# Optimization experiments

Measured on AMD Instinct MI355X. Metric: run time of the kernel, lower is better.

The kernel has to match this reference:

```python
import jax, jax.numpy as jnp
import numpy as np

B, L = 2, 2048          # batch, seq len (self-attention: M == L)
H, D, NB = 8, 16, 8     # n_heads, clifford_dim, n_blades (2^3 for sig_g=[1,1,1])
DM = H * D * NB         # d_model = 1024

# reverse() signs per blade for a 3D algebra, blade grades [0,1,1,1,2,2,2,3]:
# (-1)^{k(k-1)/2}; Euclidean metric signs from get_blade_signs are all +1,
# so the combined twist q_w = reverse(q) * signs is just these per-blade signs.
REV_SIGNS = jnp.array([1., 1., 1., 1., -1., -1., -1., -1.], dtype=jnp.float32)


def setup_inputs() -> dict:
    key = jax.random.key(0)
    ks = jax.random.split(key, 7)
    s = 1.0 / np.sqrt(DM)
    return {
        "query": jax.random.normal(ks[0], (B, L, DM), dtype=jnp.float32),
        "Wq": jax.random.normal(ks[1], (DM, DM), dtype=jnp.float32) * s,
        "bq": jax.random.normal(ks[2], (DM,), dtype=jnp.float32) * s,
        "Wk": jax.random.normal(ks[3], (DM, DM), dtype=jnp.float32) * s,
        "bk": jax.random.normal(ks[4], (DM,), dtype=jnp.float32) * s,
        "Wv": jax.random.normal(ks[5], (DM, DM), dtype=jnp.float32) * s,
        "bv": jax.random.normal(ks[6], (DM,), dtype=jnp.float32) * s,
    }


def reference(query, Wq, bq, Wk, bk, Wv, bv):
    b, l, _ = query.shape
    # projections (torch Linear: x @ W^T + b), reshape to (B,H,L,D,NB)
    def proj(x, W, bias):
        y = x @ W.T + bias
        return y.reshape(b, l, H, D, NB).transpose(0, 2, 1, 3, 4)

    q = proj(query, Wq, bq)
    k = proj(query, Wk, bk)   # self-attention: key = value = query
    v = proj(query, Wv, bv)

    q_w = q * REV_SIGNS  # reverse + blade-sign twist (elementwise over blade axis)
    scale = 1.0 / np.sqrt(D * NB)
    logits = jnp.einsum('bhldi,bhmdi->bhlm', q_w, k) * scale
    attn = jax.nn.softmax(logits, axis=-1)
    out = jnp.einsum('bhlm,bhmdi->bhldi', attn, v)
    out = out.transpose(0, 2, 1, 3, 4).reshape(b, l, -1)
    return out, attn.mean(axis=1)  # need_weights=True path
```

## Files before the change

kernel.cpp:

```cpp
#include <hip/hip_runtime.h>

typedef __attribute__((ext_vector_type(8))) __bf16 bf16x8;
typedef __attribute__((ext_vector_type(4))) __bf16 bf16x4;
typedef __attribute__((ext_vector_type(4))) float f32x4;
typedef __attribute__((ext_vector_type(16))) float f32x16;
typedef __attribute__((ext_vector_type(8))) unsigned short us8;
typedef __attribute__((ext_vector_type(4))) unsigned int u32x4;

constexpr float SCALE_L2E = 0.08838834764831845f * 1.4426950408889634f;

__device__ __forceinline__ unsigned short f2bf(float f) {
  unsigned int u = __float_as_uint(f);
  u = (u + 0x7FFFu + ((u >> 16) & 1u)) >> 16;
  return (unsigned short)u;
}

__device__ __forceinline__ void gl_lds16(const void* g, void* l) {
  __builtin_amdgcn_global_load_lds(
      (__attribute__((address_space(1))) void*)const_cast<void*>(g),
      (__attribute__((address_space(3))) void*)l, 16, 0, 0);
}

__global__ __launch_bounds__(256) void k_convert(
    const float* __restrict__ q, const float* __restrict__ wq,
    const float* __restrict__ wk, const float* __restrict__ wv,
    unsigned short* __restrict__ xb, unsigned short* __restrict__ wb) {
  long i = ((long)blockIdx.x * 256 + threadIdx.x) * 8;
  const float* s; unsigned short* d;
  if (i < 4194304)      { s = q  + i;             d = xb + i; }
  else if (i < 5242880) { s = wq + (i - 4194304); d = wb + (i - 4194304); }
  else if (i < 6291456) { s = wk + (i - 5242880); d = wb + 1048576 + (i - 5242880); }
  else                  { s = wv + (i - 6291456); d = wb + 2097152 + (i - 6291456); }
  float4 a = *(const float4*)s;
  float4 b = *(const float4*)(s + 4);
  us8 r;
  r[0]=f2bf(a.x); r[1]=f2bf(a.y); r[2]=f2bf(a.z); r[3]=f2bf(a.w);
  r[4]=f2bf(b.x); r[5]=f2bf(b.y); r[6]=f2bf(b.z); r[7]=f2bf(b.w);
  *(us8*)d = r;
}

__global__ __launch_bounds__(256) void k_proj(
    const unsigned short* __restrict__ xb, const unsigned short* __restrict__ wb,
    const float* __restrict__ bq, const float* __restrict__ bk, const float* __restrict__ bv,
    unsigned short* __restrict__ oq, unsigned short* __restrict__ ok_, unsigned short* __restrict__ vt) {
  __shared__ unsigned short As[4096];
  __shared__ unsigned short Bs[4096];
  const int t = threadIdx.x;
  const int wave = t >> 6, lane = t & 63;
  const int lrow = lane & 15, grp = lane >> 4;
  const int z = blockIdx.z;
  const unsigned short* w = wb + (size_t)z * 1048576;
  const float* bias = (z == 0) ? bq : ((z == 1) ? bk : bv);

  const unsigned short* asrc = xb + ((size_t)(blockIdx.y * 128 + (t >> 2)) * 1024 + (t & 3) * 8);
  const unsigned short* bsrc = w  + ((size_t)(blockIdx.x * 128 + (t >> 2)) * 1024 + (t & 3) * 8);

  f32x4 acc[4][4] = {};
  for (int kt = 0; kt < 32; ++kt) {
    gl_lds16(asrc + kt*32,              &As[t*8]);
    gl_lds16(asrc + kt*32 + 64*1024,    &As[2048 + t*8]);
    gl_lds16(bsrc + kt*32,              &Bs[t*8]);
    gl_lds16(bsrc + kt*32 + 64*1024,    &Bs[2048 + t*8]);
    __syncthreads();
    const int wr = wave >> 1, wc = wave & 1;
    bf16x8 af[4], bf[4];
#pragma unroll
    for (int mf = 0; mf < 4; ++mf)
      af[mf] = *(const bf16x8*)&As[(wr*64 + mf*16 + lrow)*32 + grp*8];
#pragma unroll
    for (int nf = 0; nf < 4; ++nf)
      bf[nf] = *(const bf16x8*)&Bs[(wc*64 + nf*16 + lrow)*32 + grp*8];
#pragma unroll
    for (int mf = 0; mf < 4; ++mf)
#pragma unroll
      for (int nf = 0; nf < 4; ++nf)
        acc[mf][nf] = __builtin_amdgcn_mfma_f32_16x16x32_bf16(af[mf], bf[nf], acc[mf][nf], 0, 0, 0);
    __syncthreads();
  }
  const int wr = wave >> 1, wc = wave & 1;
  if (z == 2) {
#pragma unroll
    for (int nf = 0; nf < 4; ++nf) {
      const int col = blockIdx.x*128 + wc*64 + nf*16 + lrow;
      const int h = col >> 7, dd = col & 127;
      const int dt = dd >> 5, lv = dd & 31;
      const float bsv = bias[col];
#pragma unroll
      for (int mf = 0; mf < 4; ++mf) {
        const int r0 = blockIdx.y*128 + wr*64 + mf*16 + grp*4;
        const int bb = r0 >> 11, m = r0 & 2047;
        const int mc = m >> 4, him = (m >> 3) & 1, j0 = m & 7;
        bf16x4 pv;
#pragma unroll
        for (int i = 0; i < 4; ++i) pv[i] = (__bf16)(acc[mf][nf][i] + bsv);
        const size_t off = ((((size_t)((bb*8 + h)*4 + dt))*128 + mc)*64 + lv + 32*him)*8 + j0;
        *(bf16x4*)&vt[off] = pv;
      }
    }
  } else {
    unsigned short* dst = (z == 0) ? oq : ok_;
    const float sign = (z == 0 && (lane & 7) >= 4) ? -1.0f : 1.0f;
#pragma unroll
    for (int nf = 0; nf < 4; ++nf) {
      const int col = blockIdx.x*128 + wc*64 + nf*16 + lrow;
      const float bsv = bias[col];
#pragma unroll
      for (int mf = 0; mf < 4; ++mf)
#pragma unroll
        for (int i = 0; i < 4; ++i) {
          const int row = blockIdx.y*128 + wr*64 + mf*16 + grp*4 + i;
          dst[(size_t)row*1024 + col] = f2bf((acc[mf][nf][i] + bsv) * sign);
        }
    }
  }
}

__global__ __launch_bounds__(256) void k_repack(const unsigned short* __restrict__ kws,
                                                unsigned short* __restrict__ kfrag) {
  const int c = blockIdx.x * 256 + threadIdx.x;
  const int lane = c & 63, kc = (c >> 6) & 7, mtile = (c >> 9) & 63, bh = c >> 15;
  const int b = bh >> 3, h = bh & 7;
  const int m = mtile*32 + (lane & 31);
  const int kd = kc*16 + (lane >> 5)*8;
  us8 v = *(const us8*)&kws[((size_t)(b*2048 + m))*1024 + h*128 + kd];
  *(us8*)&kfrag[(size_t)c * 8] = v;
}

__global__ __launch_bounds__(256) void k_attn_out(
    const unsigned short* __restrict__ qw, const unsigned short* __restrict__ kfrag,
    const unsigned short* __restrict__ vfrag, float* __restrict__ outp,
    float* __restrict__ rsw) {
  __shared__ __align__(16) char pool[65536];
  unsigned short (*KsL)[8192] = (unsigned short(*)[8192])pool;
  unsigned short (*VsL)[8192] = (unsigned short(*)[8192])(pool + 32768);
  float (*slab)[32][36] = (float(*)[32][36])pool;
  float (*rsred)[32] = (float(*)[32])(pool + 61440);
  float* invb = (float*)(pool + 62464);

  const int bid = blockIdx.x;
  const int xcd = bid & 7, r_ = bid >> 3;
  const int bh = (xcd << 1) | (r_ & 1);
  const int lt = r_ >> 1;
  const int b = bh >> 3, h = bh & 7;
  const int t = threadIdx.x;
  const int wave = t >> 6, lane = t & 63;
  const int mg = wave >> 1, lg = wave & 1;
  const int lm = lane & 31, hi = lane >> 5;

  bf16x8 qf[8];
  {
    const unsigned short* qp = qw + ((size_t)(b*2048 + lt*64 + lg*32 + lm))*1024
                                  + (size_t)h*128 + hi*8;
#pragma unroll
    for (int kc = 0; kc < 8; ++kc) qf[kc] = *(const bf16x8*)(qp + kc*16);
  }

  const unsigned short* kbp = kfrag + (size_t)bh*262144;
  const unsigned short* vbp = vfrag + (size_t)bh*262144;
  const int vdt = (t >> 6) & 3, vln = (t & 63) * 8;

  auto STAGE = [&](int buf, int it) {
#pragma unroll
    for (int q = 0; q < 2; ++q)
#pragma unroll
      for (int p = 0; p < 2; ++p)
        gl_lds16(kbp + (q*32 + it)*4096 + (p*256 + t)*8, &KsL[buf][q*4096 + (p*256 + t)*8]);
#pragma unroll
    for (int s = 0; s < 2; ++s)
#pragma unroll
      for (int w2 = 0; w2 < 2; ++w2)
        gl_lds16(vbp + vdt*65536 + (s*64 + it*2 + w2)*512 + vln,
                 &VsL[buf][s*4096 + w2*2048 + vdt*512 + vln]);
  };

  f32x16 oacc[4] = {};
  float rs = 0.f;

  STAGE(0, 0);
  __syncthreads();

  for (int it = 0; it < 32; ++it) {
    const int cur = it & 1;
    if (it + 1 < 32) STAGE(cur ^ 1, it + 1);

    bf16x8 kf[8];
#pragma unroll
    for (int kc = 0; kc < 8; ++kc)
      kf[kc] = *(const bf16x8*)&KsL[cur][mg*4096 + kc*512 + lane*8];
    f32x16 s = {};
#pragma unroll
    for (int kc = 0; kc < 8; ++kc)
      s = __builtin_amdgcn_mfma_f32_32x32x16_bf16(kf[kc], qf[kc], s, 0, 0, 0);

    bf16x8 vf[8];
#pragma unroll
    for (int w2 = 0; w2 < 2; ++w2)
#pragma unroll
      for (int dt = 0; dt < 4; ++dt)
        vf[w2*4 + dt] = *(const bf16x8*)&VsL[cur][mg*4096 + w2*2048 + dt*512 + lane*8];

    float e[16];
#pragma unroll
    for (int r = 0; r < 16; ++r) e[r] = __builtin_amdgcn_exp2f(s[r] * SCALE_L2E);
    float ps = 0.f;
#pragma unroll
    for (int r = 0; r < 16; ++r) ps += e[r];
    rs += ps;

    bf16x8 pf[2];
#pragma unroll
    for (int w2 = 0; w2 < 2; ++w2) {
      unsigned a0, a1, b0, b1;
      asm("v_cvt_pk_bf16_f32 %0, %1, %2" : "=v"(a0) : "v"(e[8*w2+0]), "v"(e[8*w2+1]));
      asm("v_cvt_pk_bf16_f32 %0, %1, %2" : "=v"(a1) : "v"(e[8*w2+2]), "v"(e[8*w2+3]));
      asm("v_cvt_pk_bf16_f32 %0, %1, %2" : "=v"(b0) : "v"(e[8*w2+4]), "v"(e[8*w2+5]));
      asm("v_cvt_pk_bf16_f32 %0, %1, %2" : "=v"(b1) : "v"(e[8*w2+6]), "v"(e[8*w2+7]));
      asm("v_permlane32_swap_b32 %0, %1" : "+v"(a0), "+v"(b0));
      asm("v_permlane32_swap_b32 %0, %1" : "+v"(a1), "+v"(b1));
      u32x4 pw = {a0, a1, b0, b1};
      pf[w2] = __builtin_bit_cast(bf16x8, pw);
    }

#pragma unroll
    for (int dt = 0; dt < 4; ++dt) {
      oacc[dt] = __builtin_amdgcn_mfma_f32_32x32x16_bf16(vf[dt],     pf[0], oacc[dt], 0, 0, 0);
      oacc[dt] = __builtin_amdgcn_mfma_f32_32x32x16_bf16(vf[4 + dt], pf[1], oacc[dt], 0, 0, 0);
    }
    __syncthreads();
  }

  rs += __shfl_xor(rs, 32, 64);
  if (lane < 32) rsred[wave][lm] = rs;
  __syncthreads();
  if (t < 64) {
    const int tlg = t >> 5, tl = t & 31;
    const float tot = rsred[tlg][tl] + rsred[2 + tlg][tl];
    rsw[(size_t)bh*2048 + lt*64 + t] = tot;
    invb[t] = 1.0f / tot;
  }

#pragma unroll
  for (int dt = 0; dt < 4; ++dt) {
    __syncthreads();
#pragma unroll
    for (int c = 0; c < 4; ++c) {
      float4 v4 = { oacc[dt][4*c + 0], oacc[dt][4*c + 1], oacc[dt][4*c + 2], oacc[dt][4*c + 3] };
      *(float4*)&slab[wave][lm][8*c + 4*hi] = v4;
    }
    __syncthreads();
    const int lgg = t >> 7, idx = t & 127;
    const int l = idx >> 2, d0 = (idx & 3) * 8;
    const float iv = invb[lgg*32 + l];
    float4 x0 = *(const float4*)&slab[lgg][l][d0];
    float4 x1 = *(const float4*)&slab[lgg][l][d0 + 4];
    float4 y0 = *(const float4*)&slab[2 + lgg][l][d0];
    float4 y1 = *(const float4*)&slab[2 + lgg][l][d0 + 4];
    float4 o0 = { (x0.x + y0.x)*iv, (x0.y + y0.y)*iv, (x0.z + y0.z)*iv, (x0.w + y0.w)*iv };
    float4 o1 = { (x1.x + y1.x)*iv, (x1.y + y1.y)*iv, (x1.z + y1.z)*iv, (x1.w + y1.w)*iv };
    float* op = outp + ((size_t)(b*2048 + lt*64 + lgg*32 + l))*1024 + h*128 + dt*32 + d0;
    *(float4*)op = o0;
    *(float4*)(op + 4) = o1;
  }
}

__global__ __launch_bounds__(512, 2) void k_attn_mean(
    const unsigned short* __restrict__ qw, const unsigned short* __restrict__ kfrag,
    const float* __restrict__ rsw, float* __restrict__ meanp) {
  __shared__ unsigned short KsL[2][32768];
  __shared__ unsigned int slabu[8][32][18];
  __shared__ float inv_s[512];
  const int bid = blockIdx.x;
  const int xcd = bid & 7, lt = bid >> 3;
  const int b = xcd >> 2, ms = xcd & 3;
  const int t = threadIdx.x;
  const int h = t >> 6, lane = t & 63;
  const int lm = lane & 31, hi = lane >> 5;

  inv_s[t] = 1.0f / rsw[(size_t)(b*8 + (t >> 6))*2048 + lt*64 + (t & 63)];

  bf16x8 qf0[8], qf1[8];
  {
    const unsigned short* qp0 = qw + ((size_t)(b*2048 + lt*64 + lm))*1024 + h*128 + hi*8;
#pragma unroll
    for (int kc = 0; kc < 8; ++kc) qf0[kc] = *(const bf16x8*)(qp0 + kc*16);
    const unsigned short* qp1 = qp0 + 32*1024;
#pragma unroll
    for (int kc = 0; kc < 8; ++kc) qf1[kc] = *(const bf16x8*)(qp1 + kc*16);
  }

  auto STAGE = [&](int buf, int it) {
#pragma unroll
    for (int i = 0; i < 8; ++i) {
      const int c = i*512 + t;
      const int hh = c >> 9;
      gl_lds16(kfrag + (size_t)(b*8 + hh)*262144 + (size_t)(ms*16 + it)*4096 + (c & 511)*8,
               &KsL[buf][c*8]);
    }
  };

  STAGE(0, 0);
  __syncthreads();

  float iv0[16], iv1[16];
#pragma unroll
  for (int r = 0; r < 16; ++r) {
    const int lo = (r & 3) + 8*(r >> 2) + 4*hi;
    iv0[r] = inv_s[h*64 + lo];
    iv1[r] = inv_s[h*64 + 32 + lo];
  }

  const int rm = t & 31, lp = t >> 5;

  for (int it = 0; it < 16; ++it) {
    const int cur = it & 1;
    if (it + 1 < 16) STAGE(cur ^ 1, it + 1);

    bf16x8 kf[8];
#pragma unroll
    for (int kc = 0; kc < 8; ++kc)
      kf[kc] = *(const bf16x8*)&KsL[cur][(h*8 + kc)*512 + lane*8];

    unsigned pk1[8];
    {
      f32x16 s = {};
#pragma unroll
      for (int kc = 0; kc < 8; ++kc)
        s = __builtin_amdgcn_mfma_f32_32x32x16_bf16(qf0[kc], kf[kc], s, 0, 0, 0);
#pragma unroll
      for (int gq = 0; gq < 4; ++gq) {
        float e0 = __builtin_amdgcn_exp2f(s[gq*4+0]*SCALE_L2E) * iv0[gq*4+0];
        float e1 = __builtin_amdgcn_exp2f(s[gq*4+1]*SCALE_L2E) * iv0[gq*4+1];
        float e2 = __builtin_amdgcn_exp2f(s[gq*4+2]*SCALE_L2E) * iv0[gq*4+2];
        float e3 = __builtin_amdgcn_exp2f(s[gq*4+3]*SCALE_L2E) * iv0[gq*4+3];
        unsigned p0, p1;
        asm("v_cvt_pk_bf16_f32 %0, %1, %2" : "=v"(p0) : "v"(e0), "v"(e1));
        asm("v_cvt_pk_bf16_f32 %0, %1, %2" : "=v"(p1) : "v"(e2), "v"(e3));
        uint2 w2; w2.x = p0; w2.y = p1;
        *(uint2*)&slabu[h][lm][gq*4 + hi*2] = w2;
      }
    }
    asm volatile("s_waitcnt lgkmcnt(0)" ::: "memory");
    __builtin_amdgcn_sched_barrier(0);
    __builtin_amdgcn_s_barrier();

    {
      f32x16 s = {};
#pragma unroll
      for (int kc = 0; kc < 8; ++kc)
        s = __builtin_amdgcn_mfma_f32_32x32x16_bf16(qf1[kc], kf[kc], s, 0, 0, 0);
#pragma unroll
      for (int gq = 0; gq < 4; ++gq) {
        float e0 = __builtin_amdgcn_exp2f(s[gq*4+0]*SCALE_L2E) * iv1[gq*4+0];
        float e1 = __builtin_amdgcn_exp2f(s[gq*4+1]*SCALE_L2E) * iv1[gq*4+1];
        float e2 = __builtin_amdgcn_exp2f(s[gq*4+2]*SCALE_L2E) * iv1[gq*4+2];
        float e3 = __builtin_amdgcn_exp2f(s[gq*4+3]*SCALE_L2E) * iv1[gq*4+3];
        asm("v_cvt_pk_bf16_f32 %0, %1, %2" : "=v"(pk1[gq*2+0]) : "v"(e0), "v"(e1));
        asm("v_cvt_pk_bf16_f32 %0, %1, %2" : "=v"(pk1[gq*2+1]) : "v"(e2), "v"(e3));
      }
    }
    {
      float a0 = 0.f, a1 = 0.f;
#pragma unroll
      for (int w = 0; w < 8; ++w) {
        const unsigned pv = slabu[w][rm][lp];
        a0 += __uint_as_float(pv << 16);
        a1 += __uint_as_float(pv & 0xFFFF0000u);
      }
      float* op = meanp + (size_t)(b*2048 + lt*64 + 2*lp)*2048 + (ms*16 + it)*32 + rm;
      op[0]    = a0 * 0.125f;
      op[2048] = a1 * 0.125f;
    }
    asm volatile("s_waitcnt lgkmcnt(0)" ::: "memory");
    __builtin_amdgcn_sched_barrier(0);
    __builtin_amdgcn_s_barrier();

#pragma unroll
    for (int gq = 0; gq < 4; ++gq) {
      uint2 w2; w2.x = pk1[gq*2+0]; w2.y = pk1[gq*2+1];
      *(uint2*)&slabu[h][lm][gq*4 + hi*2] = w2;
    }
    asm volatile("s_waitcnt lgkmcnt(0)" ::: "memory");
    __builtin_amdgcn_sched_barrier(0);
    __builtin_amdgcn_s_barrier();

    {
      float a0 = 0.f, a1 = 0.f;
#pragma unroll
      for (int w = 0; w < 8; ++w) {
        const unsigned pv = slabu[w][rm][lp];
        a0 += __uint_as_float(pv << 16);
        a1 += __uint_as_float(pv & 0xFFFF0000u);
      }
      float* op = meanp + (size_t)(b*2048 + lt*64 + 32 + 2*lp)*2048 + (ms*16 + it)*32 + rm;
      op[0]    = a0 * 0.125f;
      op[2048] = a1 * 0.125f;
    }
    asm volatile("s_waitcnt vmcnt(0) lgkmcnt(0)" ::: "memory");
    __builtin_amdgcn_sched_barrier(0);
    __builtin_amdgcn_s_barrier();
  }
}

extern "C" void kernel_launch(void* const* d_in, const int* in_sizes, int n_in,
                              void* d_out, int out_size, void* d_ws, size_t ws_size,
                              hipStream_t stream) {
  (void)in_sizes; (void)n_in; (void)out_size; (void)ws_size;
  const float* query = (const float*)d_in[0];
  const float* Wq = (const float*)d_in[1];
  const float* bq = (const float*)d_in[2];
  const float* Wk = (const float*)d_in[3];
  const float* bk = (const float*)d_in[4];
  const float* Wv = (const float*)d_in[5];
  const float* bv = (const float*)d_in[6];
  float* outp  = (float*)d_out;
  float* meanp = outp + 4194304;

  char* ws = (char*)d_ws;
  unsigned short* xb    = (unsigned short*)(ws);
  unsigned short* wb    = (unsigned short*)(ws + 8388608);
  unsigned short* qws   = (unsigned short*)(ws + 14680064);
  unsigned short* kws   = (unsigned short*)(ws + 23068672);
  unsigned short* kfrag = (unsigned short*)(ws + 31457280);
  unsigned short* vfrag = (unsigned short*)(ws + 39845888);
  float*          rsw   = (float*)(ws + 48234496);

  k_convert<<<3584, 256, 0, stream>>>(query, Wq, Wk, Wv, xb, wb);
  k_proj<<<dim3(8, 32, 3), 256, 0, stream>>>(xb, wb, bq, bk, bv, qws, kws, vfrag);
  k_repack<<<2048, 256, 0, stream>>>(kws, kfrag);
  k_attn_out<<<512, 256, 0, stream>>>(qws, kfrag, vfrag, outp, rsw);
  k_attn_mean<<<256, 512, 0, stream>>>(qws, kfrag, rsw, meanp);
}
```

Baseline: 137.1 us.

## Store unnormalized bf16 probabilities in attention pass and stream head-mean from workspace

The attention-output kernel now writes each tile of unnormalized bf16 exp-scores to a large workspace buffer. A new streaming kernel then averages them across heads, normalizing each by the stored row sums. This replaces the separate k_attn_mean kernel, which recomputed QK^T and exp for every head. The trade is roughly 134MB of bf16 writes plus reads in place of that recompute, and the new path only runs when the workspace is large enough.

Result: slower. 144.6 us (+5.5%).

```diff
diff --git a/kernel.cpp b/kernel.cpp
--- a/kernel.cpp
+++ b/kernel.cpp
@@ -126,10 +126,11 @@
   *(us8*)&kfrag[(size_t)c * 8] = v;
 }
 
+template<bool STOREP>
 __global__ __launch_bounds__(256) void k_attn_out(
     const unsigned short* __restrict__ qw, const unsigned short* __restrict__ kfrag,
     const unsigned short* __restrict__ vfrag, float* __restrict__ outp,
-    float* __restrict__ rsw) {
+    float* __restrict__ rsw, unsigned short* __restrict__ Pws) {
   __shared__ __align__(16) char pool[65536];
   unsigned short (*KsL)[8192] = (unsigned short(*)[8192])pool;
   unsigned short (*VsL)[8192] = (unsigned short(*)[8192])(pool + 32768);
@@ -219,6 +220,13 @@
       asm("v_permlane32_swap_b32 %0, %1" : "+v"(a1), "+v"(b1));
       u32x4 pw = {a0, a1, b0, b1};
       pf[w2] = __builtin_bit_cast(bf16x8, pw);
+    }
+
+    if constexpr (STOREP) {
+      unsigned short* pp = Pws + ((size_t)bh*2048 + lt*64 + lg*32 + lm)*2048
+                               + (size_t)(mg*32 + it)*32 + hi*8;
+      *(us8*)pp        = __builtin_bit_cast(us8, pf[0]);
+      *(us8*)(pp + 16) = __builtin_bit_cast(us8, pf[1]);
     }
 
 #pragma unroll
@@ -263,6 +271,34 @@
   }
 }
 
+__global__ __launch_bounds__(256) void k_mean_stream(
+    const unsigned short* __restrict__ Pws, const float* __restrict__ rsw,
+    float* __restrict__ meanp) {
+  const size_t gid = (size_t)blockIdx.x * 256 + threadIdx.x;
+  const int mc = (int)(gid & 127);
+  const int l  = (int)((gid >> 7) & 2047);
+  const int b  = (int)(gid >> 18);
+  float acc[16] = {};
+#pragma unroll
+  for (int h = 0; h < 8; ++h) {
+    const unsigned short* pp = Pws + ((size_t)(b*8 + h)*2048 + l)*2048 + mc*16;
+    us8 v0 = *(const us8*)pp;
+    us8 v1 = *(const us8*)(pp + 8);
+    const float iv = 1.0f / rsw[(size_t)(b*8 + h)*2048 + l];
+#pragma unroll
+    for (int j = 0; j < 8; ++j) {
+      acc[j]     += __uint_as_float((unsigned)v0[j] << 16) * iv;
+      acc[8 + j] += __uint_as_float((unsigned)v1[j] << 16) * iv;
+    }
+  }
+  float* op = meanp + ((size_t)(b*2048 + l))*2048 + mc*16;
+#pragma unroll
+  for (int q = 0; q < 4; ++q) {
+    float4 o = { acc[q*4+0]*0.125f, acc[q*4+1]*0.125f, acc[q*4+2]*0.125f, acc[q*4+3]*0.125f };
+    *(float4*)(op + q*4) = o;
+  }
+}
+
 __global__ __launch_bounds__(512, 2) void k_attn_mean(
     const unsigned short* __restrict__ qw, const unsigned short* __restrict__ kfrag,
     const float* __restrict__ rsw, float* __restrict__ meanp) {
@@ -404,7 +440,7 @@
 extern "C" void kernel_launch(void* const* d_in, const int* in_sizes, int n_in,
                               void* d_out, int out_size, void* d_ws, size_t ws_size,
                               hipStream_t stream) {
-  (void)in_sizes; (void)n_in; (void)out_size; (void)ws_size;
+  (void)in_sizes; (void)n_in; (void)out_size;
   const float* query = (const float*)d_in[0];
   const float* Wq = (const float*)d_in[1];
   const float* bq = (const float*)d_in[2];
@@ -423,10 +459,17 @@
   unsigned short* kfrag = (unsigned short*)(ws + 31457280);
   unsigned short* vfrag = (unsigned short*)(ws + 39845888);
   float*          rsw   = (float*)(ws + 48234496);
+  unsigned short* Pws   = (unsigned short*)(ws + 48365568);
+  const bool bigws = ws_size >= 182583296ull;
 
   k_convert<<<3584, 256, 0, stream>>>(query, Wq, Wk, Wv, xb, wb);
   k_proj<<<dim3(8, 32, 3), 256, 0, stream>>>(xb, wb, bq, bk, bv, qws, kws, vfrag);
   k_repack<<<2048, 256, 0, stream>>>(kws, kfrag);
-  k_attn_out<<<512, 256, 0, stream>>>(qws, kfrag, vfrag, outp, rsw);
-  k_attn_mean<<<256, 512, 0, stream>>>(qws, kfrag, rsw, meanp);
-}
+  if (bigws) {
+    k_attn_out<true><<<512, 256, 0, stream>>>(qws, kfrag, vfrag, outp, rsw, Pws);
+    k_mean_stream<<<2048, 256, 0, stream>>>(Pws, rsw, meanp);
+  } else {
+    k_attn_out<false><<<512, 256, 0, stream>>>(qws, kfrag, vfrag, outp, rsw, nullptr);
+    k_attn_mean<<<256, 512, 0, stream>>>(qws, kfrag, rsw, meanp);
+  }
+}
```
